# Kernel optimization log

Measured on AMD Instinct MI355X. Metric: run time of the kernel, lower is better.

## Reference

```python
import jax, jax.numpy as jnp
import numpy as np

EPS = 1e-5
SLOPE = 0.2


def knn_idx(x, k):
    # x: (B, C, N) -> idx: (B, N, k) of nearest neighbors (incl. self)
    xt = jnp.swapaxes(x, 1, 2)                      # (B, N, C)
    inner = -2.0 * jnp.einsum('bnc,bmc->bnm', xt, xt)
    xx = jnp.sum(x * x, axis=1)                     # (B, N)
    pd = -xx[:, :, None] - inner - xx[:, None, :]   # -squared distance
    return jax.lax.top_k(pd, k)[1]


def graph_feature(x, k):
    # x: (B, C, N) -> (B, 2C, N, k) edge features [x_j - x_i, x_i]
    B, C, N = x.shape
    idx = knn_idx(x, k)                              # (B, N, k)
    xt = jnp.swapaxes(x, 1, 2)                       # (B, N, C)
    nbr = jax.vmap(lambda a, i: a[i])(xt, idx)       # (B, N, k, C)
    ctr = xt[:, :, None, :]                          # (B, N, 1, C)
    out = jnp.concatenate([nbr - ctr, jnp.broadcast_to(ctr, (B, N, k, C))], axis=-1)
    return jnp.transpose(out, (0, 3, 1, 2))          # (B, 2C, N, k)


def batchnorm(h, g, b, axes):
    # training-mode BN: batch stats over `axes`, channel axis = 1
    m = jnp.mean(h, axes, keepdims=True)
    v = jnp.var(h, axes, keepdims=True)
    bshape = (1, -1) + (1,) * (h.ndim - 2)
    return (h - m) / jnp.sqrt(v + EPS) * g.reshape(bshape) + b.reshape(bshape)


def leaky(h):
    return jnp.where(h >= 0, h, SLOPE * h)


def edge_block(x, W, g, b, k):
    f = graph_feature(x, k)                          # (B, 2C, N, k)
    h = jnp.einsum('oc,bcnk->bonk', W, f)            # 1x1 conv2d, no bias
    h = leaky(batchnorm(h, g, b, (0, 2, 3)))
    return jnp.max(h, axis=-1)                       # max over k -> (B, O, N)


def setup_inputs() -> dict:
    key = jax.random.key(0)
    ks = jax.random.split(key, 16)
    x = jax.random.normal(ks[0], (8, 3, 2048), dtype=jnp.float32)
    def w(kk, o, c):
        return jax.random.normal(kk, (o, c), dtype=jnp.float32) * (1.0 / np.sqrt(c))
    inp = {'x': x, 'k': 20}
    dims = [(64, 6), (64, 128), (128, 128), (256, 256), (512, 512)]
    for i, (o, c) in enumerate(dims, start=1):
        inp[f'W{i}'] = w(ks[i], o, c)
        inp[f'g{i}'] = jnp.ones((o,), dtype=jnp.float32)
        inp[f'b{i}'] = jnp.zeros((o,), dtype=jnp.float32)
    return inp


def reference(x, k, W1, g1, b1, W2, g2, b2, W3, g3, b3, W4, g4, b4, W5, g5, b5):
    x1 = edge_block(x, W1, g1, b1, k)    # (B, 64, N)
    x2 = edge_block(x1, W2, g2, b2, k)   # (B, 64, N)
    x3 = edge_block(x2, W3, g3, b3, k)   # (B, 128, N)
    x4 = edge_block(x3, W4, g4, b4, k)   # (B, 256, N)
    xc = jnp.concatenate([x1, x2, x3, x4], axis=1)   # (B, 512, N)
    h = jnp.einsum('oc,bcn->bon', W5, xc)            # 1x1 conv1d
    h = leaky(batchnorm(h, g5, b5, (0, 2)))          # (B, 512, N)
    mx = jnp.max(h, axis=-1)
    av = jnp.mean(h, axis=-1)
    return jnp.concatenate([mx, av], axis=1)         # (B, 1024)
```

## Files before the change

### kernel.cpp

```cpp
#include <hip/hip_runtime.h>
#include <math.h>
#include <stdint.h>

#define B_ 8
#define N_ 2048
#define K_ 20
#define EPSV 1e-5f
#define SLOPEV 0.2f
#define TP_ 16
#define NCOPY 32

typedef unsigned short u16;
typedef unsigned long long u64;
typedef __attribute__((ext_vector_type(8))) short s8v;
typedef __attribute__((ext_vector_type(4))) float f4v;

static __device__ __forceinline__ float leakyf(float v){ return v >= 0.f ? v : SLOPEV*v; }

static __device__ __forceinline__ u16 f2bf(float f){
  unsigned u = __float_as_uint(f);
  return (u16)((u + 0x7fffu + ((u >> 16) & 1u)) >> 16);
}
static __device__ __forceinline__ float bf2f(u16 h){ return __uint_as_float(((unsigned)h) << 16); }

static __device__ __forceinline__ unsigned fkey(float f){
  unsigned u = __float_as_uint(f);
  return u ^ ((u >> 31) ? 0xFFFFFFFFu : 0x80000000u);
}

__global__ void k_transpose_in(const float* __restrict__ x, float* __restrict__ xt){
  int id = blockIdx.x*256 + threadIdx.x;
  if (id >= B_*N_) return;
  int b = id / N_, n = id % N_;
  float4 z0, z1 = {0.f,0.f,0.f,0.f};
  z0.x = x[((size_t)b*3+0)*N_ + n];
  z0.y = x[((size_t)b*3+1)*N_ + n];
  z0.z = x[((size_t)b*3+2)*N_ + n];
  z0.w = 0.f;
  ((float4*)&xt[(size_t)id*8])[0] = z0;
  ((float4*)&xt[(size_t)id*8])[1] = z1;
}

__global__ void k_prep_w(const float* __restrict__ W, float* __restrict__ Wa,
                         float* __restrict__ Wd, int O, int C){
  int id = blockIdx.x*256 + threadIdx.x;
  if (id >= O*C) return;
  int o = id / C, c = id % C;
  float a = W[(size_t)o*2*C + c];
  float d = W[(size_t)o*2*C + C + c];
  Wa[id] = a; Wd[id] = d - a;
}

__global__ void k_sqnorm(const float* __restrict__ X, int ld, int C, float* __restrict__ xx){
  int id = blockIdx.x*256 + threadIdx.x;
  if (id >= B_*N_) return;
  const float* p = X + (size_t)id*ld;
  float s = 0.f;
  for (int c = 0; c < C; ++c) s = fmaf(p[c], p[c], s);
  xx[id] = s;
}

__global__ void k_cvt3(const float* __restrict__ in, int ld, int Cin, int Cout,
                       u16* __restrict__ ph, u16* __restrict__ pm, u16* __restrict__ pl,
                       int total){
  int id = blockIdx.x*256 + threadIdx.x;
  if (id >= total) return;
  int r = id / Cout, c = id % Cout;
  float x = (c < Cin) ? in[(size_t)r*ld + c] : 0.f;
  u16 h = f2bf(x);
  float r1 = x - bf2f(h);
  u16 m = f2bf(r1);
  float r2 = r1 - bf2f(m);
  ph[id] = h; pm[id] = m; pl[id] = f2bf(r2);
}

__global__ void k_cvt2(const float* __restrict__ in, int ld, int Cin, int Cout,
                       u16* __restrict__ ph, u16* __restrict__ pm, int total){
  int id = blockIdx.x*256 + threadIdx.x;
  if (id >= total) return;
  int r = id / Cout, c = id % Cout;
  float x = (c < Cin) ? in[(size_t)r*ld + c] : 0.f;
  u16 h = f2bf(x);
  ph[id] = h;
  pm[id] = f2bf(x - bf2f(h));
}

__global__ void k_bn_cvt3(float* __restrict__ xcs, int Cout,
                          const float* __restrict__ sc, const float* __restrict__ sh,
                          u16* __restrict__ ph, u16* __restrict__ pm, u16* __restrict__ pl,
                          int total){
  int id = blockIdx.x*256 + threadIdx.x;
  if (id >= total) return;
  int r = id / Cout, c = id % Cout;
  float* p = &xcs[(size_t)r*512 + c];
  float x = leakyf(fmaf(*p, sc[c], sh[c]));
  *p = x;
  u16 h = f2bf(x);
  float r1 = x - bf2f(h);
  u16 m = f2bf(r1);
  float r2 = r1 - bf2f(m);
  ph[id] = h; pm[id] = m; pl[id] = f2bf(r2);
}

#define MT 128
#define KT 32
#define LDT 40

template<int MODE, int NPL>
__global__ __launch_bounds__(256)
void k_mfma_nt(const u16* __restrict__ Ah, const u16* __restrict__ Am, const u16* __restrict__ Al, long sA,
               const u16* __restrict__ Bh, const u16* __restrict__ Bm, const u16* __restrict__ Bl, long sB,
               float* __restrict__ Cm, int ldc, long sC, int K,
               const float* __restrict__ xx, long sX){
  __shared__ __align__(16) u16 As[NPL][MT][LDT];
  __shared__ __align__(16) u16 Bs[NPL][MT][LDT];
  const int z = blockIdx.z;
  int bx = blockIdx.x, by = blockIdx.y;
  if (MODE == 1){
    int tt = blockIdx.x, bi = 0;
    while (tt >= 16 - bi){ tt -= 16 - bi; ++bi; }
    bx = bi; by = bi + tt;
  }
  const int m0 = bx*MT, n0 = by*MT;
  const int t = threadIdx.x;
  const int lane = t & 63, wv = t >> 6;
  const int wm = (wv >> 1)*64, wn = (wv & 1)*64;
  const int lr = lane & 15, lg = lane >> 4;

  const u16* gsrc[4*NPL];
  u16* ldst[4*NPL];
  #pragma unroll
  for (int s = 0; s < 4*NPL; ++s){
    int f = s*256 + t;
    int p = f >> 9;
    int r = (f >> 2) & 127;
    int g = f & 3;
    const u16* base;
    int row0;
    u16* lb;
    if (p < NPL){
      base = ((p == 0) ? Ah : (p == 1) ? Am : Al) + (size_t)z*sA;
      row0 = m0;
      lb = &As[p][0][0];
    } else {
      int pb = p - NPL;
      base = ((pb == 0) ? Bh : (pb == 1) ? Bm : Bl) + (size_t)z*sB;
      row0 = n0;
      lb = &Bs[pb][0][0];
    }
    gsrc[s] = base + (size_t)(row0 + r)*K + g*8;
    ldst[s] = lb + r*LDT + g*8;
  }

  f4v acc[4][4] = {};

  s8v st[4*NPL];
  #pragma unroll
  for (int s = 0; s < 4*NPL; ++s) st[s] = *(const s8v*)(gsrc[s]);

  for (int k0 = 0; k0 < K; k0 += KT){
    __syncthreads();
    #pragma unroll
    for (int s = 0; s < 4*NPL; ++s) *(s8v*)(ldst[s]) = st[s];
    __syncthreads();
    if (k0 + KT < K){
      #pragma unroll
      for (int s = 0; s < 4*NPL; ++s) st[s] = *(const s8v*)(gsrc[s] + k0 + KT);
    }
    s8v bh[4], bm[4], bl[4];
    #pragma unroll
    for (int j = 0; j < 4; ++j){
      int rb = wn + j*16 + lr;
      bh[j] = *(const s8v*)&Bs[0][rb][lg*8];
      bm[j] = *(const s8v*)&Bs[1][rb][lg*8];
      if constexpr (NPL == 3) bl[j] = *(const s8v*)&Bs[2][rb][lg*8];
    }
    #pragma unroll
    for (int i = 0; i < 4; ++i){
      int ra = wm + i*16 + lr;
      s8v ah = *(const s8v*)&As[0][ra][lg*8];
      s8v am = *(const s8v*)&As[1][ra][lg*8];
      s8v al;
      if constexpr (NPL == 3) al = *(const s8v*)&As[2][ra][lg*8];
      #pragma unroll
      for (int j = 0; j < 4; ++j){
        acc[i][j] = __builtin_amdgcn_mfma_f32_16x16x32_bf16(ah, bh[j], acc[i][j], 0, 0, 0);
        acc[i][j] = __builtin_amdgcn_mfma_f32_16x16x32_bf16(ah, bm[j], acc[i][j], 0, 0, 0);
        acc[i][j] = __builtin_amdgcn_mfma_f32_16x16x32_bf16(am, bh[j], acc[i][j], 0, 0, 0);
        if constexpr (NPL == 3){
          acc[i][j] = __builtin_amdgcn_mfma_f32_16x16x32_bf16(am, bm[j], acc[i][j], 0, 0, 0);
          acc[i][j] = __builtin_amdgcn_mfma_f32_16x16x32_bf16(ah, bl[j], acc[i][j], 0, 0, 0);
          acc[i][j] = __builtin_amdgcn_mfma_f32_16x16x32_bf16(al, bh[j], acc[i][j], 0, 0, 0);
        }
      }
    }
  }

  float* Cb = Cm + (size_t)z*sC;
  float xn[4], xmr[4][4];
  if (MODE == 1){
    const float* xb = xx + (size_t)z*sX;
    #pragma unroll
    for (int j = 0; j < 4; ++j) xn[j] = xb[n0 + wn + j*16 + lr];
    #pragma unroll
    for (int i = 0; i < 4; ++i)
      #pragma unroll
      for (int q = 0; q < 4; ++q)
        xmr[i][q] = xb[m0 + wm + i*16 + lg*4 + q];
  }
  #pragma unroll
  for (int i = 0; i < 4; ++i){
    #pragma unroll
    for (int q = 0; q < 4; ++q){
      int m = m0 + wm + i*16 + lg*4 + q;
      #pragma unroll
      for (int j = 0; j < 4; ++j){
        int n = n0 + wn + j*16 + lr;
        float v = acc[i][j][q];
        if (MODE == 1) v = 2.f*v - xmr[i][q] - xn[j];
        if (MODE == 2) v += Cb[(size_t)m*ldc + n];
        Cb[(size_t)m*ldc + n] = v;
      }
    }
  }

  if (MODE == 1 && bx != by){
    float* T = (float*)&As[0][0][0];
    #pragma unroll
    for (int p = 0; p < 2; ++p){
      __syncthreads();
      #pragma unroll
      for (int jj = 0; jj < 2; ++jj){
        int j = 2*p + jj;
        int tr = (wn >> 1) + 16*jj + lr;
        #pragma unroll
        for (int i = 0; i < 4; ++i){
          float4 v4;
          v4.x = 2.f*acc[i][j][0] - xmr[i][0] - xn[j];
          v4.y = 2.f*acc[i][j][1] - xmr[i][1] - xn[j];
          v4.z = 2.f*acc[i][j][2] - xmr[i][2] - xn[j];
          v4.w = 2.f*acc[i][j][3] - xmr[i][3] - xn[j];
          *(float4*)&T[(size_t)tr*132 + wm + i*16 + lg*4] = v4;
        }
      }
      __syncthreads();
      #pragma unroll
      for (int w8 = 0; w8 < 8; ++w8){
        int f = w8*256 + t;
        int r = f >> 5;
        int cg = f & 31;
        int n = n0 + ((r >> 5) << 6) + p*32 + (r & 31);
        float4 v = *(float4*)&T[(size_t)r*132 + cg*4];
        *(float4*)&Cb[(size_t)n*ldc + m0 + cg*4] = v;
      }
    }
  }
}

__global__ __launch_bounds__(256)
void k_topk(const float* __restrict__ pd, int b0, int* __restrict__ idx){
  __shared__ u64 skey[4][64];
  const int w = threadIdx.x >> 6, lane = threadIdx.x & 63;
  const int row = blockIdx.x*4 + w;
  const float* prow = pd + (size_t)row * N_;

  float e[32];
  #pragma unroll
  for (int q = 0; q < 8; ++q){
    float4 v4 = ((const float4*)prow)[q*64 + lane];
    e[4*q+0] = v4.x; e[4*q+1] = v4.y; e[4*q+2] = v4.z; e[4*q+3] = v4.w;
  }

  float lmax = e[0];
  #pragma unroll
  for (int q = 1; q < 32; ++q) lmax = fmaxf(lmax, e[q]);

  float sv = lmax;
  #pragma unroll
  for (int k = 2; k <= 64; k <<= 1){
    #pragma unroll
    for (int j = k >> 1; j > 0; j >>= 1){
      float o = __shfl_xor(sv, j);
      bool keepMax = (((lane & k) == 0) == ((lane & j) != 0));
      sv = keepMax ? fmaxf(sv, o) : fminf(sv, o);
    }
  }
  float t = __shfl(sv, 40);

  const u64 below = (lane == 0) ? 0ULL : (~0ULL >> (64 - lane));
  int base = 0;
  #pragma unroll
  for (int q = 0; q < 32; ++q){
    bool pred = e[q] > t;
    u64 mask = __ballot(pred);
    if (pred){
      int p = base + __popcll(mask & below);
      if (p < 64){
        int ei = (q>>2)*256 + lane*4 + (q&3);
        skey[w][p] = ((u64)fkey(e[q]) << 32) | (unsigned)(N_ - 1 - ei);
      }
    }
    base += __popcll(mask);
  }
  int C = base;
  asm volatile("s_waitcnt lgkmcnt(0)" ::: "memory");

  const int gb = b0 + row / N_;
  const int n = row % N_;
  int* out = idx + ((size_t)gb*N_ + n)*K_;

  if (C >= K_ && C <= 64){
    u64 key = (lane < C) ? skey[w][lane] : 0ULL;
    #pragma unroll
    for (int k = 2; k <= 64; k <<= 1){
      #pragma unroll
      for (int j = k >> 1; j > 0; j >>= 1){
        u64 o = __shfl_xor(key, j);
        bool keepMax = (((lane & k) == 0) == ((lane & j) != 0));
        bool sel = (key > o) == keepMax;
        key = sel ? key : o;
      }
    }
    if (lane >= 44) out[63 - lane] = (N_ - 1) - (int)(key & 0xFFFFFFFFu);
  } else {
    for (int tt = 0; tt < K_; ++tt){
      float best = -INFINITY; int bi = 0x7FFFFFFF;
      #pragma unroll
      for (int q = 0; q < 32; ++q){
        int iq = (q>>2)*256 + lane*4 + (q&3);
        if (e[q] > best || (e[q] == best && iq < bi)){ best = e[q]; bi = iq; }
      }
      #pragma unroll
      for (int off = 32; off; off >>= 1){
        float ov = __shfl_xor(best, off);
        int oi = __shfl_xor(bi, off);
        if (ov > best || (ov == best && oi < bi)){ best = ov; bi = oi; }
      }
      if (lane == 0) out[tt] = bi;
      #pragma unroll
      for (int q = 0; q < 32; ++q){
        int iq = (q>>2)*256 + lane*4 + (q&3);
        if (iq == bi) e[q] = -INFINITY;
      }
    }
  }
}

__global__ __launch_bounds__(256)
void k_edge_assemble(const float* __restrict__ uv, const int* __restrict__ idx,
                     float* __restrict__ xc, int O, int c0,
                     float* __restrict__ ssum, float* __restrict__ ssq){
  const int tid = threadIdx.x;
  const int npar = 256 / O;
  const int o = tid % O;
  const int slot = tid / O;
  const int b = blockIdx.x & 7;
  const int tile = blockIdx.x >> 3;
  const int ld = 2*O;
  float lsum = 0.f, lsq = 0.f;
  for (int i = slot; i < TP_; i += npar){
    int n = tile*TP_ + i;
    const float vv = uv[((size_t)b*N_+n)*ld + O + o];
    const int* ip = idx + ((size_t)b*N_+n)*K_;
    float m = -INFINITY;
    #pragma unroll
    for (int kk = 0; kk < K_; ++kk){
      int j = ip[kk];
      float h = uv[((size_t)b*N_+j)*ld + o] + vv;
      m = fmaxf(m, h);
      lsum += h;
      lsq = fmaf(h, h, lsq);
    }
    xc[((size_t)b*N_+n)*512 + c0 + o] = m;
  }
  const int cp = blockIdx.x & (NCOPY-1);
  atomicAdd(&ssum[cp*O + o], lsum);
  atomicAdd(&ssq[cp*O + o], lsq);
}

__global__ void k_bn_finalize(const float* __restrict__ ssum, const float* __restrict__ ssq,
                              const float* __restrict__ g, const float* __restrict__ bb,
                              float* __restrict__ sc, float* __restrict__ sh, int O, double cnt){
  int o = threadIdx.x;
  if (o >= O) return;
  double S1 = 0.0, S2 = 0.0;
  for (int c = 0; c < NCOPY; ++c){
    S1 += (double)ssum[c*O + o];
    S2 += (double)ssq[c*O + o];
  }
  double mean = S1 / cnt;
  double var = S2 / cnt - mean*mean;
  if (var < 0.0) var = 0.0;
  float inv = rsqrtf((float)var + EPSV);
  float s = g[o] * inv;
  sc[o] = s;
  sh[o] = bb[o] - (float)mean * s;
}

__global__ void k_bn_apply(float* __restrict__ xc, int O, int c0,
                           const float* __restrict__ sc, const float* __restrict__ sh){
  int id = blockIdx.x*256 + threadIdx.x;
  if (id >= B_*N_*O) return;
  int o = id % O;
  size_t pn = (size_t)(id / O);
  float* p = &xc[pn*512 + c0 + o];
  float val = fmaf(*p, sc[o], sh[o]);
  *p = leakyf(val);
}

__global__ void k_h5_stats(const float* __restrict__ h5, float* __restrict__ ssum, float* __restrict__ ssq){
  const int o = threadIdx.x;
  const int nb = N_/64;
  const int b = blockIdx.x / nb, tile = blockIdx.x % nb;
  float ls = 0.f, lq = 0.f;
  for (int i = 0; i < 64; ++i){
    float v = h5[((size_t)b*N_ + tile*64 + i)*512 + o];
    ls += v;
    lq = fmaf(v, v, lq);
  }
  const int cp = blockIdx.x & (NCOPY-1);
  atomicAdd(&ssum[cp*512 + o], ls);
  atomicAdd(&ssq[cp*512 + o], lq);
}

__global__ void k_final_partial(const float* __restrict__ h5, const float* __restrict__ sc,
                                const float* __restrict__ sh, float* __restrict__ pmax,
                                float* __restrict__ psum){
  const int o = threadIdx.x;
  const int b = blockIdx.x >> 4, c = blockIdx.x & 15;
  const float s = sc[o], t = sh[o];
  float mx = -INFINITY, sm = 0.f;
  for (int i = 0; i < 128; ++i){
    int n = c*128 + i;
    float v = leakyf(fmaf(h5[((size_t)b*N_+n)*512 + o], s, t));
    mx = fmaxf(mx, v);
    sm += v;
  }
  pmax[(size_t)blockIdx.x*512 + o] = mx;
  psum[(size_t)blockIdx.x*512 + o] = sm;
}

__global__ void k_final_combine(const float* __restrict__ pmax, const float* __restrict__ psum,
                                float* __restrict__ out){
  const int o = threadIdx.x;
  const int b = blockIdx.x;
  float mx = -INFINITY, sm = 0.f;
  for (int c = 0; c < 16; ++c){
    mx = fmaxf(mx, pmax[((size_t)b*16+c)*512 + o]);
    sm += psum[((size_t)b*16+c)*512 + o];
  }
  out[(size_t)b*1024 + o] = mx;
  out[(size_t)b*1024 + 512 + o] = sm * (1.f/N_);
}

extern "C" void kernel_launch(void* const* d_in, const int* in_sizes, int n_in,
                              void* d_out, int out_size, void* d_ws, size_t ws_size,
                              hipStream_t stream){
  const float* x  = (const float*)d_in[0];
  const float* W1 = (const float*)d_in[2];
  const float* g1 = (const float*)d_in[3];
  const float* b1 = (const float*)d_in[4];
  const float* W2 = (const float*)d_in[5];
  const float* g2 = (const float*)d_in[6];
  const float* b2 = (const float*)d_in[7];
  const float* W3 = (const float*)d_in[8];
  const float* g3 = (const float*)d_in[9];
  const float* b3 = (const float*)d_in[10];
  const float* W4 = (const float*)d_in[11];
  const float* g4 = (const float*)d_in[12];
  const float* b4 = (const float*)d_in[13];
  const float* W5 = (const float*)d_in[14];
  const float* g5 = (const float*)d_in[15];
  const float* b5 = (const float*)d_in[16];
  float* out = (float*)d_out;

  size_t fixed_f = (size_t)B_*N_*512*2 + (size_t)B_*N_ + 2u*256*128 + 2u*512 + 2u*NCOPY*512;
  size_t need4 = (fixed_f + (size_t)4*N_*N_)*4 + (size_t)B_*N_*K_*4;
  const int NB = (ws_size >= need4) ? 4 : 2;
  const size_t RFLOATS = (size_t)NB*N_*N_;

  float* w = (float*)d_ws;
  float* xc  = w; w += (size_t)B_*N_*512;
  float* h5  = w; w += (size_t)B_*N_*512;
  float* R   = w; w += RFLOATS;
  float* xx  = w; w += (size_t)B_*N_;
  float* Wa  = w; w += 256*128;
  float* Wd  = w; w += 256*128;
  float* sc  = w; w += 512;
  float* sh  = w; w += 512;
  float* ssum = w; w += (size_t)NCOPY*512;
  float* ssq  = w; w += (size_t)NCOPY*512;
  int* idxp  = (int*)w; w += (size_t)B_*N_*K_;
  (void)in_sizes; (void)n_in; (void)out_size;

  float* x0t = h5;
  u16* Xh = (u16*)(h5 + 131072);
  u16* Xm = Xh + 2097152;
  u16* Xl = Xm + 2097152;
  u16* WhE = Xl + 2097152;
  u16* WmE = WhE + 65536;
  u16* WlE = WmE + 65536;
  float* uv = R;
  float* pmax = R;
  float* psum = R + 128*512;

  k_transpose_in<<<dim3((B_*N_)/256), dim3(256), 0, stream>>>(x, x0t);

  struct Cfg { const float* Xin; int lda; int Cw; int Cout;
               const float* W; const float* g; const float* bb; int O; int c0; };
  Cfg cfgs[4] = {
    { x0t,      8,   3,   32,  W1, g1, b1, 64,  0   },
    { xc + 0,   512, 64,  64,  W2, g2, b2, 64,  64  },
    { xc + 64,  512, 64,  64,  W3, g3, b3, 128, 128 },
    { xc + 128, 512, 128, 128, W4, g4, b4, 256, 256 },
  };

  for (int e = 0; e < 4; ++e){
    Cfg c = cfgs[e];
    k_prep_w<<<dim3((c.O*c.Cw + 255)/256), dim3(256), 0, stream>>>(c.W, Wa, Wd, c.O, c.Cw);
    k_sqnorm<<<dim3((B_*N_)/256), dim3(256), 0, stream>>>(c.Xin, c.lda, c.Cw, xx);
    if (e == 0){
      int totX = B_*N_*c.Cout;
      k_cvt3<<<dim3((totX + 255)/256), dim3(256), 0, stream>>>(c.Xin, c.lda, c.Cw, c.Cout, Xh, Xm, Xl, totX);
    }
    long sAb = (long)N_*c.Cout;
    for (int b0 = 0; b0 < B_; b0 += NB){
      const u16* Ah = Xh + (size_t)b0*sAb;
      const u16* Am = Xm + (size_t)b0*sAb;
      const u16* Al = Xl + (size_t)b0*sAb;
      k_mfma_nt<1,3><<<dim3(136,1,NB), dim3(256), 0, stream>>>(
          Ah, Am, Al, sAb, Ah, Am, Al, sAb,
          R, N_, (long)N_*N_, c.Cout, xx + b0*N_, (long)N_);
      k_topk<<<dim3((NB*N_)/4), dim3(256), 0, stream>>>(R, b0, idxp);
    }
    int totW = c.O*c.Cout;
    k_cvt3<<<dim3((totW + 255)/256), dim3(256), 0, stream>>>(Wa, c.Cw, c.Cw, c.Cout, WhE, WmE, WlE, totW);
    k_cvt3<<<dim3((totW + 255)/256), dim3(256), 0, stream>>>(Wd, c.Cw, c.Cw, c.Cout,
        WhE + totW, WmE + totW, WlE + totW, totW);
    int twoO = 2*c.O;
    k_mfma_nt<0,3><<<dim3(16, twoO/128, 8), dim3(256), 0, stream>>>(
        Xh, Xm, Xl, sAb, WhE, WmE, WlE, 0L,
        uv, twoO, (long)N_*twoO, c.Cout, nullptr, 0L);
    hipMemsetAsync(ssum, 0, (size_t)NCOPY*512*sizeof(float), stream);
    hipMemsetAsync(ssq, 0, (size_t)NCOPY*512*sizeof(float), stream);
    k_edge_assemble<<<dim3(B_*(N_/TP_)), dim3(256), 0, stream>>>(uv, idxp, xc, c.O, c.c0, ssum, ssq);
    k_bn_finalize<<<dim3(1), dim3(512), 0, stream>>>(ssum, ssq, c.g, c.bb, sc, sh, c.O, (double)B_*N_*K_);
    if (e < 3){
      int totN = B_*N_*cfgs[e+1].Cout;
      k_bn_cvt3<<<dim3((totN + 255)/256), dim3(256), 0, stream>>>(
          xc + c.c0, cfgs[e+1].Cout, sc, sh, Xh, Xm, Xl, totN);
    } else {
      k_bn_apply<<<dim3((B_*N_*c.O)/256), dim3(256), 0, stream>>>(xc, c.O, c.c0, sc, sh);
    }
  }

  if (NB == 4){
    u16* Rh = (u16*)R;
    u16* Rm = Rh + 8388608;
    u16* W5h = Rm + 8388608;
    u16* W5m = W5h + 262144;
    k_cvt2<<<dim3((B_*N_*512)/256), dim3(256), 0, stream>>>(xc, 512, 512, 512, Rh, Rm, B_*N_*512);
    k_cvt2<<<dim3((512*512)/256), dim3(256), 0, stream>>>(W5, 512, 512, 512, W5h, W5m, 512*512);
    k_mfma_nt<0,2><<<dim3(16, 4, 8), dim3(256), 0, stream>>>(
        Rh, Rm, nullptr, (long)N_*512, W5h, W5m, nullptr, 0L,
        h5, 512, (long)N_*512, 512, nullptr, 0L);
  } else {
    u16* Rh = (u16*)R;
    u16* Rm = Rh + 4194304;
    u16* W5h = Rm + 4194304;
    u16* W5m = W5h + 131072;
    for (int hf = 0; hf < 2; ++hf){
      int totA = B_*N_*256;
      k_cvt2<<<dim3((totA)/256), dim3(256), 0, stream>>>(xc + hf*256, 512, 256, 256, Rh, Rm, totA);
      k_cvt2<<<dim3((512*256)/256), dim3(256), 0, stream>>>(W5 + hf*256, 512, 256, 256, W5h, W5m, 512*256);
      if (hf == 0)
        k_mfma_nt<0,2><<<dim3(16, 4, 8), dim3(256), 0, stream>>>(
            Rh, Rm, nullptr, (long)N_*256, W5h, W5m, nullptr, 0L,
            h5, 512, (long)N_*512, 256, nullptr, 0L);
      else
        k_mfma_nt<2,2><<<dim3(16, 4, 8), dim3(256), 0, stream>>>(
            Rh, Rm, nullptr, (long)N_*256, W5h, W5m, nullptr, 0L,
            h5, 512, (long)N_*512, 256, nullptr, 0L);
    }
  }
  hipMemsetAsync(ssum, 0, (size_t)NCOPY*512*sizeof(float), stream);
  hipMemsetAsync(ssq, 0, (size_t)NCOPY*512*sizeof(float), stream);
  k_h5_stats<<<dim3(B_*(N_/64)), dim3(512), 0, stream>>>(h5, ssum, ssq);
  k_bn_finalize<<<dim3(1), dim3(512), 0, stream>>>(ssum, ssq, g5, b5, sc, sh, 512, (double)B_*N_);
  k_final_partial<<<dim3(B_*16), dim3(512), 0, stream>>>(h5, sc, sh, pmax, psum);
  k_final_combine<<<dim3(B_), dim3(512), 0, stream>>>(pmax, psum, out);
}
```

Baseline: 695.6 us.

## Fuse final BN stats into GEMM epilogue, fold BN4 into conversion, allow NB=8

Drops the separate layer-4 BN-apply pass and instead applies BN and leaky to channels 256+ inside the bf16 split conversion feeding the final conv. Computes the per-channel sum and sum-of-squares for the final BN inside the GEMM epilogue with atomics, which removes the k_h5_stats pass over h5. It also adds an NB=8 option so all batches' distance matrices are processed in one launch when the workspace is large enough. The trade-off is that xc for layer 4 is never written back in normalized form, plus extra atomics and register use in the GEMM epilogue.

Result: faster. 640.0 us (-8.0%).

```diff
diff --git a/kernel.cpp b/kernel.cpp
--- a/kernel.cpp
+++ b/kernel.cpp
@@ -74,12 +74,14 @@
   ph[id] = h; pm[id] = m; pl[id] = f2bf(r2);
 }
 
-__global__ void k_cvt2(const float* __restrict__ in, int ld, int Cin, int Cout,
-                       u16* __restrict__ ph, u16* __restrict__ pm, int total){
+__global__ void k_bn_cvt2(const float* __restrict__ in, int ld, int Cin, int Cout, int cthr,
+                          const float* __restrict__ sc, const float* __restrict__ sh,
+                          u16* __restrict__ ph, u16* __restrict__ pm, int total){
   int id = blockIdx.x*256 + threadIdx.x;
   if (id >= total) return;
   int r = id / Cout, c = id % Cout;
   float x = (c < Cin) ? in[(size_t)r*ld + c] : 0.f;
+  if (c >= cthr) x = leakyf(fmaf(x, sc[c - cthr], sh[c - cthr]));
   u16 h = f2bf(x);
   ph[id] = h;
   pm[id] = f2bf(x - bf2f(h));
@@ -111,7 +113,8 @@
 void k_mfma_nt(const u16* __restrict__ Ah, const u16* __restrict__ Am, const u16* __restrict__ Al, long sA,
                const u16* __restrict__ Bh, const u16* __restrict__ Bm, const u16* __restrict__ Bl, long sB,
                float* __restrict__ Cm, int ldc, long sC, int K,
-               const float* __restrict__ xx, long sX){
+               const float* __restrict__ xx, long sX,
+               float* __restrict__ ssum, float* __restrict__ ssq){
   __shared__ __align__(16) u16 As[NPL][MT][LDT];
   __shared__ __align__(16) u16 Bs[NPL][MT][LDT];
   const int z = blockIdx.z;
@@ -208,6 +211,7 @@
       for (int q = 0; q < 4; ++q)
         xmr[i][q] = xb[m0 + wm + i*16 + lg*4 + q];
   }
+  float ls[4] = {0.f,0.f,0.f,0.f}, lq[4] = {0.f,0.f,0.f,0.f};
   #pragma unroll
   for (int i = 0; i < 4; ++i){
     #pragma unroll
@@ -220,7 +224,17 @@
         if (MODE == 1) v = 2.f*v - xmr[i][q] - xn[j];
         if (MODE == 2) v += Cb[(size_t)m*ldc + n];
         Cb[(size_t)m*ldc + n] = v;
-      }
+        if (MODE >= 2){ ls[j] += v; lq[j] = fmaf(v, v, lq[j]); }
+      }
+    }
+  }
+  if (MODE >= 2){
+    int cp = ((blockIdx.x << 3) + blockIdx.z) & (NCOPY-1);
+    #pragma unroll
+    for (int j = 0; j < 4; ++j){
+      int n = n0 + wn + j*16 + lr;
+      atomicAdd(&ssum[cp*512 + n], ls[j]);
+      atomicAdd(&ssq[cp*512 + n], lq[j]);
     }
   }
 
@@ -395,32 +409,6 @@
   float s = g[o] * inv;
   sc[o] = s;
   sh[o] = bb[o] - (float)mean * s;
-}
-
-__global__ void k_bn_apply(float* __restrict__ xc, int O, int c0,
-                           const float* __restrict__ sc, const float* __restrict__ sh){
-  int id = blockIdx.x*256 + threadIdx.x;
-  if (id >= B_*N_*O) return;
-  int o = id % O;
-  size_t pn = (size_t)(id / O);
-  float* p = &xc[pn*512 + c0 + o];
-  float val = fmaf(*p, sc[o], sh[o]);
-  *p = leakyf(val);
-}
-
-__global__ void k_h5_stats(const float* __restrict__ h5, float* __restrict__ ssum, float* __restrict__ ssq){
-  const int o = threadIdx.x;
-  const int nb = N_/64;
-  const int b = blockIdx.x / nb, tile = blockIdx.x % nb;
-  float ls = 0.f, lq = 0.f;
-  for (int i = 0; i < 64; ++i){
-    float v = h5[((size_t)b*N_ + tile*64 + i)*512 + o];
-    ls += v;
-    lq = fmaf(v, v, lq);
-  }
-  const int cp = blockIdx.x & (NCOPY-1);
-  atomicAdd(&ssum[cp*512 + o], ls);
-  atomicAdd(&ssq[cp*512 + o], lq);
 }
 
 __global__ void k_final_partial(const float* __restrict__ h5, const float* __restrict__ sc,
@@ -475,8 +463,10 @@
   float* out = (float*)d_out;
 
   size_t fixed_f = (size_t)B_*N_*512*2 + (size_t)B_*N_ + 2u*256*128 + 2u*512 + 2u*NCOPY*512;
-  size_t need4 = (fixed_f + (size_t)4*N_*N_)*4 + (size_t)B_*N_*K_*4;
-  const int NB = (ws_size >= need4) ? 4 : 2;
+  size_t idxb = (size_t)B_*N_*K_*4;
+  size_t need8 = (fixed_f + (size_t)8*N_*N_)*4 + idxb;
+  size_t need4 = (fixed_f + (size_t)4*N_*N_)*4 + idxb;
+  const int NB = (ws_size >= need8) ? 8 : (ws_size >= need4) ? 4 : 2;
   const size_t RFLOATS = (size_t)NB*N_*N_;
 
   float* w = (float*)d_ws;
@@ -530,7 +520,7 @@
       const u16* Al = Xl + (size_t)b0*sAb;
       k_mfma_nt<1,3><<<dim3(136,1,NB), dim3(256), 0, stream>>>(
           Ah, Am, Al, sAb, Ah, Am, Al, sAb,
-          R, N_, (long)N_*N_, c.Cout, xx + b0*N_, (long)N_);
+          R, N_, (long)N_*N_, c.Cout, xx + b0*N_, (long)N_, nullptr, nullptr);
       k_topk<<<dim3((NB*N_)/4), dim3(256), 0, stream>>>(R, b0, idxp);
     }
     int totW = c.O*c.Cout;
@@ -540,7 +530,7 @@
     int twoO = 2*c.O;
     k_mfma_nt<0,3><<<dim3(16, twoO/128, 8), dim3(256), 0, stream>>>(
         Xh, Xm, Xl, sAb, WhE, WmE, WlE, 0L,
-        uv, twoO, (long)N_*twoO, c.Cout, nullptr, 0L);
+        uv, twoO, (long)N_*twoO, c.Cout, nullptr, 0L, nullptr, nullptr);
     hipMemsetAsync(ssum, 0, (size_t)NCOPY*512*sizeof(float), stream);
     hipMemsetAsync(ssq, 0, (size_t)NCOPY*512*sizeof(float), stream);
     k_edge_assemble<<<dim3(B_*(N_/TP_)), dim3(256), 0, stream>>>(uv, idxp, xc, c.O, c.c0, ssum, ssq);
@@ -549,21 +539,23 @@
       int totN = B_*N_*cfgs[e+1].Cout;
       k_bn_cvt3<<<dim3((totN + 255)/256), dim3(256), 0, stream>>>(
           xc + c.c0, cfgs[e+1].Cout, sc, sh, Xh, Xm, Xl, totN);
-    } else {
-      k_bn_apply<<<dim3((B_*N_*c.O)/256), dim3(256), 0, stream>>>(xc, c.O, c.c0, sc, sh);
-    }
-  }
-
-  if (NB == 4){
+    }
+  }
+
+  hipMemsetAsync(ssum, 0, (size_t)NCOPY*512*sizeof(float), stream);
+  hipMemsetAsync(ssq, 0, (size_t)NCOPY*512*sizeof(float), stream);
+  if (NB >= 4){
     u16* Rh = (u16*)R;
     u16* Rm = Rh + 8388608;
     u16* W5h = Rm + 8388608;
     u16* W5m = W5h + 262144;
-    k_cvt2<<<dim3((B_*N_*512)/256), dim3(256), 0, stream>>>(xc, 512, 512, 512, Rh, Rm, B_*N_*512);
-    k_cvt2<<<dim3((512*512)/256), dim3(256), 0, stream>>>(W5, 512, 512, 512, W5h, W5m, 512*512);
-    k_mfma_nt<0,2><<<dim3(16, 4, 8), dim3(256), 0, stream>>>(
+    k_bn_cvt2<<<dim3((B_*N_*512)/256), dim3(256), 0, stream>>>(
+        xc, 512, 512, 512, 256, sc, sh, Rh, Rm, B_*N_*512);
+    k_bn_cvt2<<<dim3((512*512)/256), dim3(256), 0, stream>>>(
+        W5, 512, 512, 512, 512, nullptr, nullptr, W5h, W5m, 512*512);
+    k_mfma_nt<3,2><<<dim3(16, 4, 8), dim3(256), 0, stream>>>(
         Rh, Rm, nullptr, (long)N_*512, W5h, W5m, nullptr, 0L,
-        h5, 512, (long)N_*512, 512, nullptr, 0L);
+        h5, 512, (long)N_*512, 512, nullptr, 0L, ssum, ssq);
   } else {
     u16* Rh = (u16*)R;
     u16* Rm = Rh + 4194304;
@@ -571,21 +563,20 @@
     u16* W5m = W5h + 131072;
     for (int hf = 0; hf < 2; ++hf){
       int totA = B_*N_*256;
-      k_cvt2<<<dim3((totA)/256), dim3(256), 0, stream>>>(xc + hf*256, 512, 256, 256, Rh, Rm, totA);
-      k_cvt2<<<dim3((512*256)/256), dim3(256), 0, stream>>>(W5 + hf*256, 512, 256, 256, W5h, W5m, 512*256);
+      k_bn_cvt2<<<dim3((totA)/256), dim3(256), 0, stream>>>(
+          xc + hf*256, 512, 256, 256, (hf == 0) ? 256 : 0, sc, sh, Rh, Rm, totA);
+      k_bn_cvt2<<<dim3((512*256)/256), dim3(256), 0, stream>>>(
+          W5 + hf*256, 512, 256, 256, 256, nullptr, nullptr, W5h, W5m, 512*256);
       if (hf == 0)
         k_mfma_nt<0,2><<<dim3(16, 4, 8), dim3(256), 0, stream>>>(
             Rh, Rm, nullptr, (long)N_*256, W5h, W5m, nullptr, 0L,
-            h5, 512, (long)N_*512, 256, nullptr, 0L);
+            h5, 512, (long)N_*512, 256, nullptr, 0L, nullptr, nullptr);
       else
         k_mfma_nt<2,2><<<dim3(16, 4, 8), dim3(256), 0, stream>>>(
             Rh, Rm, nullptr, (long)N_*256, W5h, W5m, nullptr, 0L,
-            h5, 512, (long)N_*512, 256, nullptr, 0L);
-    }
-  }
-  hipMemsetAsync(ssum, 0, (size_t)NCOPY*512*sizeof(float), stream);
-  hipMemsetAsync(ssq, 0, (size_t)NCOPY*512*sizeof(float), stream);
-  k_h5_stats<<<dim3(B_*(N_/64)), dim3(512), 0, stream>>>(h5, ssum, ssq);
+            h5, 512, (long)N_*512, 256, nullptr, 0L, ssum, ssq);
+    }
+  }
   k_bn_finalize<<<dim3(1), dim3(512), 0, stream>>>(ssum, ssq, g5, b5, sc, sh, 512, (double)B_*N_);
   k_final_partial<<<dim3(B_*16), dim3(512), 0, stream>>>(h5, sc, sh, pmax, psum);
   k_final_combine<<<dim3(B_), dim3(512), 0, stream>>>(pmax, psum, out);
```
